# Kernel tuning notes

Measured on AMD Instinct MI355X. Metric: run time of the kernel, lower is better.

The kernel has to match this reference:

```python
import jax, jax.numpy as jnp
import numpy as np

N_PROT = 100_000; E_PROT = 1_600_000
N_LIG = 5_000;    E_LIG = 80_000
B_PROT = 64; B_LIG = 1
SEQ = 130; D = 45; K = 4; DIN = 74
PROT_DIMS = [DIN, 50, 45, 45]
LIG_DIMS  = [DIN, 50, 45, 45, 45]
HEAD = [SEQ * D, 2000, 1000, 500, 1]


def setup_inputs() -> dict:
    key = jax.random.key(0)
    ks = iter(jax.random.split(key, 64))
    def rn(shape, scale=1.0):
        return jax.random.normal(next(ks), shape, jnp.float32) * scale
    inp = {
        "prot_x": rn((N_PROT, DIN)),
        "lig_x": rn((N_LIG, DIN)),
    }
    for pref, dims in (("prot", PROT_DIMS), ("lig", LIG_DIMS)):
        for i in range(len(dims) - 1):
            fan_in = (K + 1) * dims[i]
            inp[f"{pref}_W{i}"] = rn((fan_in, dims[i + 1]), fan_in ** -0.5)
            inp[f"{pref}_b{i}"] = jnp.zeros((dims[i + 1],), jnp.float32)
    inp["qkv_w"] = rn((D, 3 * D), D ** -0.5)
    inp["qkv_b"] = jnp.zeros((3 * D,), jnp.float32)
    inp["proj_w"] = rn((D, D), D ** -0.5)
    inp["proj_b"] = jnp.zeros((D,), jnp.float32)
    for i in range(3):
        inp[f"h{i}_w"] = rn((HEAD[i], HEAD[i + 1]), HEAD[i] ** -0.5)
        inp[f"h{i}_b"] = jnp.zeros((HEAD[i + 1],), jnp.float32)
    inp["fc_w"] = rn((HEAD[3], HEAD[4]), HEAD[3] ** -0.5)
    inp["fc_b"] = jnp.zeros((HEAD[4],), jnp.float32)
    inp["prot_src"] = jax.random.randint(next(ks), (E_PROT,), 0, N_PROT, jnp.int32)
    inp["prot_dst"] = jax.random.randint(next(ks), (E_PROT,), 0, N_PROT, jnp.int32)
    # deterministic contiguous subgraph ids guarantee all 64 pockets are non-empty
    inp["prot_gid"] = (jnp.arange(N_PROT) * B_PROT // N_PROT).astype(jnp.int32)
    inp["lig_src"] = jax.random.randint(next(ks), (E_LIG,), 0, N_LIG, jnp.int32)
    inp["lig_dst"] = jax.random.randint(next(ks), (E_LIG,), 0, N_LIG, jnp.int32)
    inp["lig_gid"] = jnp.zeros((N_LIG,), jnp.int32)
    inp["training"] = 0
    return inp


def _tagconv(x, src, dst, W, b, n):
    # DGL TAGConv: h_{k+1} = D^{-1/2} A D^{-1/2} h_k ; out = [h_0..h_K] @ W + b
    deg = jax.ops.segment_sum(jnp.ones_like(dst, x.dtype), dst, num_segments=n)
    norm = jnp.where(deg > 0, deg, 1.0) ** -0.5  # clamp(min=1)^-0.5
    hops = [x]
    h = x
    for _ in range(K):
        h = norm[:, None] * jax.ops.segment_sum((h * norm[:, None])[src], dst, num_segments=n)
        hops.append(h)
    return jnp.concatenate(hops, axis=-1) @ W + b


def _l2norm(x):
    # F.normalize(dim=1): x / max(||x||_2, eps)
    return x / jnp.maximum(jnp.linalg.norm(x, axis=1, keepdims=True), 1e-12)


def _gnn(x, src, dst, gid, Ws, bs, n, ngraphs):
    for W, b in zip(Ws, bs):
        x = _l2norm(jax.nn.relu(_tagconv(x, src, dst, W, b, n)))
        # dropout is identity in eval mode
    return jax.ops.segment_max(x, gid, num_segments=ngraphs)  # DGL MaxPooling


def reference(prot_x, lig_x,
              prot_W0, prot_b0, prot_W1, prot_b1, prot_W2, prot_b2,
              lig_W0, lig_b0, lig_W1, lig_b1, lig_W2, lig_b2, lig_W3, lig_b3,
              qkv_w, qkv_b, proj_w, proj_b,
              h0_w, h0_b, h1_w, h1_b, h2_w, h2_b, fc_w, fc_b,
              prot_src, prot_dst, prot_gid, lig_src, lig_dst, lig_gid, training):
    prot_rep = _gnn(prot_x, prot_src, prot_dst, prot_gid,
                    [prot_W0, prot_W1, prot_W2], [prot_b0, prot_b1, prot_b2],
                    N_PROT, B_PROT)                    # [B_PROT, 45]
    lig_rep = _gnn(lig_x, lig_src, lig_dst, lig_gid,
                   [lig_W0, lig_W1, lig_W2, lig_W3], [lig_b0, lig_b1, lig_b2, lig_b3],
                   N_LIG, B_LIG)                       # [B_LIG, 45]
    n_seq = B_LIG + B_PROT
    seq = jnp.concatenate([lig_rep, prot_rep], axis=0)  # [n_seq, 45]
    seq = jnp.pad(seq, ((0, SEQ - n_seq), (0, 0)))[None]  # [1, 130, 45]

    # eye-based mask exactly as the torch code builds it
    idx = jnp.arange(SEQ)
    valid = idx < n_seq
    mask = jnp.eye(SEQ, dtype=jnp.float32) * (valid[:, None] & valid[None, :])
    mask = mask.at[:, n_seq - 1].set(1.0)
    mask = mask.at[n_seq - 1, :].set(1.0)
    mask = mask.at[n_seq - 1, n_seq - 1].set(0.0)

    qkv = seq @ qkv_w + qkv_b                 # [1, 130, 135]
    q, k, v = jnp.split(qkv, 3, axis=-1)      # single head, head_dim = 45
    attn = jnp.einsum("bqd,bkd->bqk", q, k) * (D ** -0.5)
    attn = jnp.where(mask[None] == 0, -1e9, attn)
    attn = jax.nn.softmax(attn, axis=-1)
    out = jnp.einsum("bqk,bkd->bqd", attn, v) @ proj_w + proj_b  # [1,130,45]

    out = out.reshape(1, SEQ * D)             # [1, 5850]
    for w, b in ((h0_w, h0_b), (h1_w, h1_b), (h2_w, h2_b)):
        out = jax.nn.relu(out @ w + b)        # head dropout off in eval
    return jax.nn.sigmoid(out @ fc_w + fc_b)  # [1, 1]
```

## Files before the change

### kernel.cpp

```cpp
#include <hip/hip_runtime.h>
#include <hip/hip_fp16.h>
#include <cstddef>
#include <cstdint>

namespace {

constexpr int NPROT = 100000;
constexpr int EPROT = 1600000;
constexpr int NLIG  = 5000;
constexpr int ELIG  = 80000;


__global__ void hist_kernel(const int* __restrict__ dst, int* __restrict__ cnt, int e) {
  int i = blockIdx.x * 256 + threadIdx.x;
  if (i < e) atomicAdd(&cnt[dst[i]], 1);
}

__global__ void scan1_kernel(const int* __restrict__ cnt, int* __restrict__ rp,
                             int* __restrict__ bsum, float* __restrict__ nrm, int n) {
  __shared__ int wsum[4];
  int t = threadIdx.x;
  int base = blockIdx.x * 1024 + t * 4;
  int v0 = 0, v1 = 0, v2 = 0, v3 = 0;
  if (base + 3 < n) {
    int4 val = *(const int4*)(cnt + base);
    v0 = val.x; v1 = val.y; v2 = val.z; v3 = val.w;
  } else if (base < n) {
    v0 = cnt[base];
    if (base + 1 < n) v1 = cnt[base + 1];
    if (base + 2 < n) v2 = cnt[base + 2];
  }
  if (base < n)     nrm[base]     = 1.0f / sqrtf(fmaxf((float)v0, 1.0f));
  if (base + 1 < n) nrm[base + 1] = 1.0f / sqrtf(fmaxf((float)v1, 1.0f));
  if (base + 2 < n) nrm[base + 2] = 1.0f / sqrtf(fmaxf((float)v2, 1.0f));
  if (base + 3 < n) nrm[base + 3] = 1.0f / sqrtf(fmaxf((float)v3, 1.0f));
  int ts = v0 + v1 + v2 + v3;
  int lane = t & 63, wv = t >> 6;
  int incl = ts;
  #pragma unroll
  for (int off = 1; off < 64; off <<= 1) {
    int o = __shfl_up(incl, off, 64);
    if (lane >= off) incl += o;
  }
  if (lane == 63) wsum[wv] = incl;
  __syncthreads();
  int woff = 0;
  #pragma unroll
  for (int i = 0; i < 4; ++i) if (i < wv) woff += wsum[i];
  int excl = woff + incl - ts;
  int o0 = excl, o1 = o0 + v0, o2 = o1 + v1, o3 = o2 + v2;
  if (base + 3 < n) {
    *(int4*)(rp + base) = make_int4(o0, o1, o2, o3);
  } else if (base < n) {
    rp[base] = o0;
    if (base + 1 < n) rp[base + 1] = o1;
    if (base + 2 < n) rp[base + 2] = o2;
  }
  if (t == 255) bsum[blockIdx.x] = woff + incl;
}

__global__ void scan2_kernel(int* __restrict__ bsum, int nb, int* __restrict__ rp_end) {
  __shared__ int s[256];
  int t = threadIdx.x;
  int v = (t < nb) ? bsum[t] : 0;
  s[t] = v;
  __syncthreads();
  int val = v;
  for (int off = 1; off < 256; off <<= 1) {
    int add = (t >= off) ? s[t - off] : 0;
    __syncthreads();
    val += add;
    s[t] = val;
    __syncthreads();
  }
  if (t < nb) bsum[t] = val - v;
  if (t == 255) *rp_end = val;
}

__global__ void scan3_kernel(int* __restrict__ rp, const int* __restrict__ bsum, int n) {
  int i = blockIdx.x * 256 + threadIdx.x;
  if (i < n) rp[i] += bsum[i >> 10];
}

__global__ void scatter_kernel(const int* __restrict__ src, const int* __restrict__ dst,
                               const int* __restrict__ rp, int* __restrict__ cur,
                               int* __restrict__ col, int e) {
  int i = blockIdx.x * 256 + threadIdx.x;
  if (i < e) {
    int d = dst[i];
    int p = rp[d] + atomicAdd(&cur[d], 1);
    col[p] = src[i];
  }
}


__global__ void gather_all_kernel(const __half* __restrict__ gin, const int* __restrict__ rp,
                                  const int* __restrict__ col, const float* __restrict__ nrm,
                                  __half* __restrict__ gout, int n, int nbn) {
  int pass = blockIdx.x / nbn;
  int bid = blockIdx.x - pass * nbn;
  int lane = threadIdx.x & 63, wv = threadIdx.x >> 6;
  int q = lane >> 4, r = lane & 15;
  int e_slot = r >> 3, f2 = r & 7;
  int v = bid * 16 + wv * 4 + q;
  bool vok = (v < n);
  int beg = 0, deg = 0;
  if (vok) { beg = rp[v]; deg = rp[v + 1] - beg; }
  const __half* gc = gin + (size_t)pass * n * 16;
  __half* go = gout + (size_t)pass * n * 16;
  float ax = 0.f, ay = 0.f;
  for (int base = 0; __any(base < deg); base += 16) {
    int ec = (base + r < deg) ? col[beg + base + r] : -1;
    #pragma unroll
    for (int js = 0; js < 16; js += 2) {
      int sl = (q << 4) + js + e_slot;
      int s0 = __shfl(ec, sl, 64);
      int idx = (s0 >= 0) ? s0 : 0;
      float m = (s0 >= 0) ? 1.f : 0.f;
      __half2 h2 = *(const __half2*)(gc + (size_t)idx * 16 + (f2 << 1));
      ax += m * __low2float(h2);
      ay += m * __high2float(h2);
    }
  }
  ax += __shfl_xor(ax, 8, 64);
  ay += __shfl_xor(ay, 8, 64);
  if (vok && e_slot == 0) {
    float nm = nrm[v];
    float nm2 = nm * nm;
    *(__half2*)(go + (size_t)v * 16 + (f2 << 1)) = __floats2half2_rn(ax * nm2, ay * nm2);
  }
}

template<int DIN>
__global__ void init_g0_kernel(const float* __restrict__ x, const float* __restrict__ nrm,
                               __half* __restrict__ g0, int n) {
  constexpr int PD = (DIN + 15) & ~15;
  int lane = threadIdx.x & 63;
  int v = blockIdx.x * 4 + (threadIdx.x >> 6);
  if (v >= n) return;
  float nm = nrm[v];
  for (int f = lane; f < PD; f += 64) {
    float val = (f < DIN) ? x[(size_t)v * DIN + f] * nm : 0.f;
    g0[(((size_t)(f >> 4) * n + v) << 4) + (f & 15)] = __float2half(val);
  }
}

__global__ void padw_kernel(const float* __restrict__ W, float* __restrict__ Wp,
                            int din, int dout, int pd) {
  int i = blockIdx.x * 256 + threadIdx.x;
  int total = 5 * pd * dout;
  if (i >= total) return;
  int f = i / dout, j = i - f * dout;
  int hop = f / pd, rem = f - hop * pd;
  Wp[i] = (rem < din) ? W[(size_t)(hop * din + rem) * dout + j] : 0.f;
}

template<int DIN, int DOUT, bool LAST>
__global__ __launch_bounds__(256) void combine_kernel(
    const __half* __restrict__ gbase, const float* __restrict__ nrm,
    const float* __restrict__ Wp, const float* __restrict__ bias,
    __half* __restrict__ gnext, float* __restrict__ Xout, int n) {
  constexpr int PD = (DIN + 15) & ~15;
  constexpr int NCH = PD / 16;
  constexpr int PDN = (DOUT + 15) & ~15;
  int v = blockIdx.x * 256 + threadIdx.x;
  if (v >= n) return;
  const size_t slabh = (size_t)n * 80;
  float acc[DOUT];
  #pragma unroll
  for (int j = 0; j < DOUT; ++j) acc[j] = 0.f;
  const float* wr = Wp;
  for (int hop = 0; hop < 5; ++hop) {
    const __half* hrow = gbase + (size_t)hop * slabh + ((size_t)v << 4);
    for (int ch = 0; ch < NCH; ++ch) {
      float h[16];
      #pragma unroll
      for (int s2 = 0; s2 < 8; ++s2) {
        __half2 hh = *(const __half2*)(hrow + s2 * 2);
        h[2 * s2]     = __low2float(hh);
        h[2 * s2 + 1] = __high2float(hh);
      }
      #pragma unroll
      for (int s = 0; s < 16; ++s) {
        #pragma unroll
        for (int j = 0; j < DOUT; ++j) acc[j] += h[s] * wr[s * DOUT + j];
      }
      wr += 16 * DOUT;
      hrow += ((size_t)n << 4);
    }
  }
  float rn = 1.f / nrm[v];
  float ss = 0.f;
  #pragma unroll
  for (int j = 0; j < DOUT; ++j) {
    float y = bias[j] + acc[j] * rn;
    y = fmaxf(y, 0.f);
    acc[j] = y;
    ss += y * y;
  }
  float sc = 1.f / fmaxf(sqrtf(ss), 1e-12f);
  if (LAST) {
    #pragma unroll
    for (int j = 0; j < DOUT; ++j) Xout[(size_t)v * DOUT + j] = acc[j] * sc;
  } else {
    float nm = nrm[v];
    #pragma unroll
    for (int ch = 0; ch < PDN / 16; ++ch) {
      __half* go = gnext + (((size_t)ch * n + v) << 4);
      #pragma unroll
      for (int s2 = 0; s2 < 8; ++s2) {
        int j0 = ch * 16 + s2 * 2, j1 = j0 + 1;
        float a = (j0 < DOUT) ? acc[j0] * sc * nm : 0.f;
        float b = (j1 < DOUT) ? acc[j1] * sc * nm : 0.f;
        *(__half2*)(go + s2 * 2) = __floats2half2_rn(a, b);
      }
    }
  }
}


template<int DIN, int GS, int DOUT>
__global__ void init_gemm_kernel(const float* __restrict__ x, const float* __restrict__ nrm,
                                 const float* __restrict__ W, const float* __restrict__ bias,
                                 __half* __restrict__ gout, float* __restrict__ y, int n) {
  int lane = threadIdx.x & 63;
  int v = blockIdx.x * 4 + (threadIdx.x >> 6);
  if (v >= n) return;
  float nm = nrm[v];
  const float* xr = x + (size_t)v * DIN;
  float hA = (lane < DIN) ? xr[lane] : 0.f;
  float hB = 0.f;
  if constexpr (DIN > 64) { if (lane + 64 < DIN) hB = xr[lane + 64]; }
  __half* go = gout + (size_t)v * GS;
  if (lane < DIN) go[lane] = __float2half(hA * nm);
  if constexpr (DIN > 64) { if (lane + 64 < DIN) go[lane + 64] = __float2half(hB * nm); }
  int cl = (lane < DOUT) ? lane : 0;
  float acc = bias[cl];
  const float* Wk = W + cl;
  #pragma unroll
  for (int f = 0; f < DIN; ++f) {
    float hf = (f < 64) ? __shfl(hA, f, 64) : __shfl(hB, f - 64, 64);
    acc += hf * Wk[(size_t)f * DOUT];
  }
  if (lane < DOUT) y[(size_t)v * DOUT + lane] = acc;
}

template<int DIN, int GS, int DOUT, bool WRITEG, bool FINAL>
__global__ void fused_hop_kernel(const __half* __restrict__ gin, const int* __restrict__ rp,
                                 const int* __restrict__ col, const float* __restrict__ nrm,
                                 const float* __restrict__ W, __half* __restrict__ gout,
                                 float* __restrict__ y, float* __restrict__ Xout,
                                 int k, int n) {
  int lane = threadIdx.x & 63;
  int v = blockIdx.x * 4 + (threadIdx.x >> 6);
  if (v >= n) return;
  int beg = rp[v], end = rp[v + 1];
  float a0 = 0.f, a1 = 0.f;
  for (int base = beg; base < end; base += 64) {
    int m = end - base; if (m > 64) m = 64;
    int myc = (lane < m) ? col[base + lane] : 0;
    int j = 0;
    for (; j + 8 <= m; j += 8) {
      int ss[8];
      float t0[8], t1[8];
      #pragma unroll
      for (int u = 0; u < 8; ++u) ss[u] = __shfl(myc, j + u, 64);
      #pragma unroll
      for (int u = 0; u < 8; ++u) {
        const __half* rr = gin + (size_t)ss[u] * GS;
        t0[u] = (lane < DIN) ? __half2float(rr[lane]) : 0.f;
        if constexpr (DIN > 64) t1[u] = (lane + 64 < DIN) ? __half2float(rr[lane + 64]) : 0.f;
      }
      #pragma unroll
      for (int u = 0; u < 8; ++u) {
        a0 += t0[u];
        if constexpr (DIN > 64) a1 += t1[u];
      }
    }
    for (; j < m; ++j) {
      int s = __shfl(myc, j, 64);
      const __half* rr = gin + (size_t)s * GS;
      if (lane < DIN) a0 += __half2float(rr[lane]);
      if constexpr (DIN > 64) { if (lane + 64 < DIN) a1 += __half2float(rr[lane + 64]); }
    }
  }
  float nm = nrm[v];
  float hA = a0 * nm, hB = a1 * nm;
  if (WRITEG) {
    __half* go = gout + (size_t)v * GS;
    if (lane < DIN) go[lane] = __float2half(hA * nm);
    if constexpr (DIN > 64) { if (lane + 64 < DIN) go[lane + 64] = __float2half(hB * nm); }
  }
  int cl = (lane < DOUT) ? lane : 0;
  float acc = 0.f;
  if (lane < DOUT) acc = y[(size_t)v * DOUT + lane];
  const float* Wk = W + (size_t)k * DIN * DOUT + cl;
  #pragma unroll
  for (int f = 0; f < DIN; ++f) {
    float hf = (f < 64) ? __shfl(hA, f, 64) : __shfl(hB, f - 64, 64);
    acc += hf * Wk[(size_t)f * DOUT];
  }
  if constexpr (FINAL) {
    float val = (lane < DOUT) ? fmaxf(acc, 0.f) : 0.f;
    float ss2 = val * val;
    #pragma unroll
    for (int off2 = 32; off2 > 0; off2 >>= 1) ss2 += __shfl_xor(ss2, off2, 64);
    float scale = 1.f / fmaxf(sqrtf(ss2), 1e-12f);
    if (lane < DOUT) Xout[(size_t)v * DOUT + lane] = val * scale;
  } else {
    if (lane < DOUT) y[(size_t)v * DOUT + lane] = acc;
  }
}

__global__ void segmax_kernel(const float* __restrict__ X, const int* __restrict__ gid,
                              float* __restrict__ rep, int n, int row_off) {
  __shared__ float tab[4][45];
  __shared__ int gids[256];
  int t = threadIdx.x;
  for (int i = t; i < 4 * 45; i += 256) ((float*)tab)[i] = 0.f;
  int v0 = blockIdx.x * 256;
  int vend = v0 + 256; if (vend > n) vend = n;
  int nv = vend - v0;
  if (t < nv) gids[t] = gid[v0 + t];
  __syncthreads();
  int g0 = gids[0];
  int total = nv * 45;
  for (int i = t; i < total; i += 256) {
    int vl = i / 45, j = i - vl * 45;
    float val = X[(size_t)(v0 + vl) * 45 + j];
    int rel = gids[vl] - g0;
    if (rel >= 0 && rel < 4)
      atomicMax((unsigned int*)&tab[rel][j], __float_as_uint(val));
    else
      atomicMax((unsigned int*)&rep[(size_t)(row_off + gids[vl]) * 45 + j], __float_as_uint(val));
  }
  __syncthreads();
  for (int i = t; i < 4 * 45; i += 256) {
    float val = ((float*)tab)[i];
    if (val > 0.f) {
      int rel = i / 45, j = i - rel * 45;
      atomicMax((unsigned int*)&rep[(size_t)(row_off + g0 + rel) * 45 + j], __float_as_uint(val));
    }
  }
}


__global__ void qkv_kernel(const float* __restrict__ rep, const float* __restrict__ w,
                           const float* __restrict__ b, float* __restrict__ qkv) {
  int i = blockIdx.x;
  int t = threadIdx.x;
  __shared__ float sr[45];
  if (t < 45) sr[t] = (i < 65) ? rep[(size_t)i * 45 + t] : 0.f;
  __syncthreads();
  if (t < 135) {
    float acc = b[t];
    #pragma unroll 5
    for (int d = 0; d < 45; ++d) acc += sr[d] * w[d * 135 + t];
    qkv[(size_t)i * 135 + t] = acc;
  }
}

__global__ void attn_kernel(const float* __restrict__ qkv, const float* __restrict__ proj_w,
                            const float* __restrict__ proj_b, float* __restrict__ ctx) {
  int i = blockIdx.x;
  int t = threadIdx.x;
  __shared__ float q[45];
  __shared__ float p[130];
  __shared__ float red[256];
  __shared__ float ao[45];
  if (t < 45) q[t] = qkv[(size_t)i * 135 + t];
  __syncthreads();
  float s = -1e30f;
  if (t < 130) {
    int j = t;
    float dot = 0.f;
    #pragma unroll 5
    for (int d = 0; d < 45; ++d) dot += q[d] * qkv[(size_t)j * 135 + 45 + d];
    dot *= 0.14907119849998599f;
    bool mz;
    if (i == 64 && j == 64) mz = true;
    else if (i == 64 || j == 64) mz = false;
    else mz = !(i == j && i < 65);
    s = mz ? -1e9f : dot;
  }
  red[t] = s;
  __syncthreads();
  #pragma unroll
  for (int off = 128; off > 0; off >>= 1) {
    if (t < off) red[t] = fmaxf(red[t], red[t + off]);
    __syncthreads();
  }
  float mx = red[0];
  __syncthreads();
  float e = (t < 130) ? expf(s - mx) : 0.f;
  red[t] = e;
  __syncthreads();
  #pragma unroll
  for (int off = 128; off > 0; off >>= 1) {
    if (t < off) red[t] += red[t + off];
    __syncthreads();
  }
  float denom = red[0];
  __syncthreads();
  if (t < 130) p[t] = e / denom;
  __syncthreads();
  if (t < 45) {
    float acc = 0.f;
    for (int j = 0; j < 130; ++j) acc += p[j] * qkv[(size_t)j * 135 + 90 + t];
    ao[t] = acc;
  }
  __syncthreads();
  if (t < 45) {
    float pr = proj_b[t];
    #pragma unroll 5
    for (int e2 = 0; e2 < 45; ++e2) pr += ao[e2] * proj_w[e2 * 45 + t];
    ctx[(size_t)i * 45 + t] = pr;
  }
}


__global__ void bias_init_kernel(const float* __restrict__ b, float* __restrict__ out, int n) {
  int i = blockIdx.x * 256 + threadIdx.x;
  if (i < n) out[i] = b[i];
}

template<bool RELU_IN>
__global__ void fc_splitk_kernel(const float* __restrict__ x, const float* __restrict__ W,
                                 float* __restrict__ out, int nin, int nout, int kchunk) {
  __shared__ float xs[1024];
  int k0 = blockIdx.y * kchunk;
  int k1 = k0 + kchunk; if (k1 > nin) k1 = nin;
  int len = k1 - k0;
  for (int i = threadIdx.x; i < len; i += blockDim.x) {
    float v = x[k0 + i];
    xs[i] = RELU_IN ? fmaxf(v, 0.f) : v;
  }
  __syncthreads();
  int j = blockIdx.x * blockDim.x + threadIdx.x;
  if (j < nout) {
    float acc = 0.f;
    const float* Wp = W + (size_t)k0 * nout + j;
    for (int i = 0; i < len; ++i) acc += xs[i] * Wp[(size_t)i * nout];
    atomicAdd(&out[j], acc);
  }
}

__global__ void final_fc_kernel(const float* __restrict__ x, const float* __restrict__ W,
                                const float* __restrict__ b, float* __restrict__ out) {
  __shared__ float red[512];
  int t = threadIdx.x;
  float acc = 0.f;
  if (t < 500) acc = fmaxf(x[t], 0.f) * W[t];
  red[t] = acc;
  __syncthreads();
  #pragma unroll
  for (int off = 256; off > 0; off >>= 1) {
    if (t < off) red[t] += red[t + off];
    __syncthreads();
  }
  if (t == 0) {
    float z = red[0] + b[0];
    out[0] = 1.f / (1.f + expf(-z));
  }
}


struct Bufs {
  __half* slabs;
  __half *ligA, *ligB;
  float *X, *Y, *nrm, *Wp;
  int *cnt, *cur, *rp, *col, *bsum;
};

template<int DIN, int DOUT, bool LAST>
void run_layer_prot(const Bufs& g, const float* W, const float* b, int n, hipStream_t st) {
  constexpr int PD = (DIN + 15) & ~15;
  constexpr int NPASS = PD / 16;
  int nbn = (n + 15) / 16;
  size_t slabh = (size_t)n * 80;
  for (int k = 1; k <= 4; ++k)
    gather_all_kernel<<<NPASS * nbn, 256, 0, st>>>(g.slabs + (size_t)(k - 1) * slabh,
                                                   g.rp, g.col, g.nrm,
                                                   g.slabs + (size_t)k * slabh, n, nbn);
  int wtotal = 5 * PD * DOUT;
  padw_kernel<<<(wtotal + 255) / 256, 256, 0, st>>>(W, g.Wp, DIN, DOUT, PD);
  combine_kernel<DIN, DOUT, LAST><<<(n + 255) / 256, 256, 0, st>>>(
      g.slabs, g.nrm, g.Wp, b, g.slabs, g.X, n);
}

template<int DIN, int GS, int DOUT>
void run_layer_lig(const float* xin, const Bufs& g, const float* W, const float* b,
                   int n, hipStream_t st) {
  int nb = (n + 3) / 4;
  init_gemm_kernel<DIN, GS, DOUT><<<nb, 256, 0, st>>>(xin, g.nrm, W, b, g.ligA, g.Y, n);
  const __half* gin = g.ligA;
  __half* gout = g.ligB;
  for (int k = 1; k <= 4; ++k) {
    if (k < 4)
      fused_hop_kernel<DIN, GS, DOUT, true, false><<<nb, 256, 0, st>>>(gin, g.rp, g.col, g.nrm, W, gout, g.Y, g.X, k, n);
    else
      fused_hop_kernel<DIN, GS, DOUT, false, true><<<nb, 256, 0, st>>>(gin, g.rp, g.col, g.nrm, W, gout, g.Y, g.X, 4, n);
    __half* t = (__half*)gin; gin = gout; gout = t;
  }
}

void build_csr(const int* src, const int* dst, const Bufs& g, int n, int e, hipStream_t st) {
  hipMemsetAsync(g.cnt, 0, (size_t)n * 4, st);
  hipMemsetAsync(g.cur, 0, (size_t)n * 4, st);
  hist_kernel<<<(e + 255) / 256, 256, 0, st>>>(dst, g.cnt, e);
  int nb1 = (n + 1023) / 1024;
  scan1_kernel<<<nb1, 256, 0, st>>>(g.cnt, g.rp, g.bsum, g.nrm, n);
  scan2_kernel<<<1, 256, 0, st>>>(g.bsum, nb1, g.rp + n);
  scan3_kernel<<<(n + 255) / 256, 256, 0, st>>>(g.rp, g.bsum, n);
  scatter_kernel<<<(e + 255) / 256, 256, 0, st>>>(src, dst, g.rp, g.cur, g.col, e);
}

}

extern "C" void kernel_launch(void* const* d_in, const int* in_sizes, int n_in,
                              void* d_out, int out_size, void* d_ws, size_t ws_size,
                              hipStream_t stream) {
  (void)in_sizes; (void)n_in; (void)out_size;

  const float* prot_x = (const float*)d_in[0];
  const float* lig_x  = (const float*)d_in[1];
  const float* pW[3] = {(const float*)d_in[2], (const float*)d_in[4], (const float*)d_in[6]};
  const float* pB[3] = {(const float*)d_in[3], (const float*)d_in[5], (const float*)d_in[7]};
  const float* lW[4] = {(const float*)d_in[8], (const float*)d_in[10], (const float*)d_in[12], (const float*)d_in[14]};
  const float* lB[4] = {(const float*)d_in[9], (const float*)d_in[11], (const float*)d_in[13], (const float*)d_in[15]};
  const float* qkv_w = (const float*)d_in[16];
  const float* qkv_b = (const float*)d_in[17];
  const float* proj_w = (const float*)d_in[18];
  const float* proj_b = (const float*)d_in[19];
  const float* h0_w = (const float*)d_in[20];
  const float* h0_b = (const float*)d_in[21];
  const float* h1_w = (const float*)d_in[22];
  const float* h1_b = (const float*)d_in[23];
  const float* h2_w = (const float*)d_in[24];
  const float* h2_b = (const float*)d_in[25];
  const float* fc_w = (const float*)d_in[26];
  const float* fc_b = (const float*)d_in[27];
  const int* prot_src = (const int*)d_in[28];
  const int* prot_dst = (const int*)d_in[29];
  const int* prot_gid = (const int*)d_in[30];
  const int* lig_src  = (const int*)d_in[31];
  const int* lig_dst  = (const int*)d_in[32];
  const int* lig_gid  = (const int*)d_in[33];

  char* w = (char*)d_ws;
  size_t off = 0;
  auto alloc = [&](size_t bytes) -> void* {
    void* p = w + off;
    off += (bytes + 255) & ~(size_t)255;
    return p;
  };
  __half* slabs = (__half*)alloc((size_t)5 * NPROT * 80 * 2);
  __half* ligA  = (__half*)alloc((size_t)NLIG * 96 * 2);
  __half* ligB  = (__half*)alloc((size_t)NLIG * 96 * 2);
  float* X   = (float*)alloc((size_t)NPROT * 45 * 4);
  float* Y   = (float*)alloc((size_t)NLIG * 50 * 4);
  float* nrm = (float*)alloc((size_t)NPROT * 4);
  float* Wp  = (float*)alloc((size_t)5 * 80 * 50 * 4);
  int* cnt   = (int*)alloc((size_t)NPROT * 4);
  int* cur   = (int*)alloc((size_t)NPROT * 4);
  int* rp    = (int*)alloc(((size_t)NPROT + 1) * 4);
  int* colb  = (int*)alloc((size_t)EPROT * 4);
  int* bsum  = (int*)alloc((size_t)256 * 4);
  float* rep = (float*)alloc((size_t)65 * 45 * 4);
  float* qkvb = (float*)alloc((size_t)130 * 135 * 4);
  float* ctx  = (float*)alloc((size_t)5850 * 4);
  float* hb0  = (float*)alloc((size_t)2000 * 4);
  float* hb1  = (float*)alloc((size_t)1000 * 4);
  float* hb2  = (float*)alloc((size_t)500 * 4);
  if (off > ws_size) return;

  hipMemsetAsync(rep, 0, (size_t)65 * 45 * 4, stream);

  Bufs g{slabs, ligA, ligB, X, Y, nrm, Wp, cnt, cur, rp, colb, bsum};

  build_csr(prot_src, prot_dst, g, NPROT, EPROT, stream);
  init_g0_kernel<74><<<(NPROT + 3) / 4, 256, 0, stream>>>(prot_x, g.nrm, g.slabs, NPROT);
  run_layer_prot<74, 50, false>(g, pW[0], pB[0], NPROT, stream);
  run_layer_prot<50, 45, false>(g, pW[1], pB[1], NPROT, stream);
  run_layer_prot<45, 45, true >(g, pW[2], pB[2], NPROT, stream);
  segmax_kernel<<<(NPROT + 255) / 256, 256, 0, stream>>>(g.X, prot_gid, rep, NPROT, 1);

  build_csr(lig_src, lig_dst, g, NLIG, ELIG, stream);
  run_layer_lig<74, 96, 50>(lig_x, g, lW[0], lB[0], NLIG, stream);
  run_layer_lig<50, 64, 45>(g.X, g, lW[1], lB[1], NLIG, stream);
  run_layer_lig<45, 64, 45>(g.X, g, lW[2], lB[2], NLIG, stream);
  run_layer_lig<45, 64, 45>(g.X, g, lW[3], lB[3], NLIG, stream);
  segmax_kernel<<<(NLIG + 255) / 256, 256, 0, stream>>>(g.X, lig_gid, rep, NLIG, 0);

  qkv_kernel<<<130, 256, 0, stream>>>(rep, qkv_w, qkv_b, qkvb);
  attn_kernel<<<130, 256, 0, stream>>>(qkvb, proj_w, proj_b, ctx);

  bias_init_kernel<<<8, 256, 0, stream>>>(h0_b, hb0, 2000);
  fc_splitk_kernel<false><<<dim3(8, 8), 256, 0, stream>>>(ctx, h0_w, hb0, 5850, 2000, 732);
  bias_init_kernel<<<4, 256, 0, stream>>>(h1_b, hb1, 1000);
  fc_splitk_kernel<true><<<dim3(4, 4), 256, 0, stream>>>(hb0, h1_w, hb1, 2000, 1000, 500);
  bias_init_kernel<<<2, 256, 0, stream>>>(h2_b, hb2, 500);
  fc_splitk_kernel<true><<<dim3(2, 2), 256, 0, stream>>>(hb1, h2_w, hb2, 1000, 500, 500);
  final_fc_kernel<<<1, 512, 0, stream>>>(hb2, fc_w, fc_b, (float*)d_out);
}
```

Baseline: 1.542 ms.

## Split combine output columns across waves and widen gather loads

The protein combine kernel now gives each node to four waves, each computing a quarter of the output columns. The L2-norm sum of squares is reduced through shared memory, which cuts per-thread accumulator registers and raises occupancy. The gather kernel switches from half2 to 8-byte loads, with four features per lane and four edge slots, plus an extra shuffle stage in the reduction. Each node's h rows are now read four times, once per wave, and the weight buffer gets padding for overrun reads.

```diff
diff --git a/kernel.cpp b/kernel.cpp
--- a/kernel.cpp
+++ b/kernel.cpp
@@ -94,6 +94,11 @@
 }
 
 
+__device__ __forceinline__ float2 cvt_h2(uint32_t u) {
+  __half2 h = *reinterpret_cast<__half2*>(&u);
+  return make_float2(__low2float(h), __high2float(h));
+}
+
 __global__ void gather_all_kernel(const __half* __restrict__ gin, const int* __restrict__ rp,
                                   const int* __restrict__ col, const float* __restrict__ nrm,
                                   __half* __restrict__ gout, int n, int nbn) {
@@ -101,33 +106,40 @@
   int bid = blockIdx.x - pass * nbn;
   int lane = threadIdx.x & 63, wv = threadIdx.x >> 6;
   int q = lane >> 4, r = lane & 15;
-  int e_slot = r >> 3, f2 = r & 7;
+  int e_slot = r >> 2, f4 = r & 3;
   int v = bid * 16 + wv * 4 + q;
   bool vok = (v < n);
   int beg = 0, deg = 0;
   if (vok) { beg = rp[v]; deg = rp[v + 1] - beg; }
   const __half* gc = gin + (size_t)pass * n * 16;
   __half* go = gout + (size_t)pass * n * 16;
-  float ax = 0.f, ay = 0.f;
+  float a0 = 0.f, a1 = 0.f, a2 = 0.f, a3 = 0.f;
   for (int base = 0; __any(base < deg); base += 16) {
     int ec = (base + r < deg) ? col[beg + base + r] : -1;
     #pragma unroll
-    for (int js = 0; js < 16; js += 2) {
+    for (int js = 0; js < 16; js += 4) {
       int sl = (q << 4) + js + e_slot;
       int s0 = __shfl(ec, sl, 64);
       int idx = (s0 >= 0) ? s0 : 0;
       float m = (s0 >= 0) ? 1.f : 0.f;
-      __half2 h2 = *(const __half2*)(gc + (size_t)idx * 16 + (f2 << 1));
-      ax += m * __low2float(h2);
-      ay += m * __high2float(h2);
-    }
-  }
-  ax += __shfl_xor(ax, 8, 64);
-  ay += __shfl_xor(ay, 8, 64);
+      uint2 u = *(const uint2*)(gc + (size_t)idx * 16 + (f4 << 2));
+      float2 p0 = cvt_h2(u.x), p1 = cvt_h2(u.y);
+      a0 += m * p0.x; a1 += m * p0.y; a2 += m * p1.x; a3 += m * p1.y;
+    }
+  }
+  a0 += __shfl_xor(a0, 4, 64);  a1 += __shfl_xor(a1, 4, 64);
+  a2 += __shfl_xor(a2, 4, 64);  a3 += __shfl_xor(a3, 4, 64);
+  a0 += __shfl_xor(a0, 8, 64);  a1 += __shfl_xor(a1, 8, 64);
+  a2 += __shfl_xor(a2, 8, 64);  a3 += __shfl_xor(a3, 8, 64);
   if (vok && e_slot == 0) {
     float nm = nrm[v];
     float nm2 = nm * nm;
-    *(__half2*)(go + (size_t)v * 16 + (f2 << 1)) = __floats2half2_rn(ax * nm2, ay * nm2);
+    __half2 w0 = __floats2half2_rn(a0 * nm2, a1 * nm2);
+    __half2 w1 = __floats2half2_rn(a2 * nm2, a3 * nm2);
+    uint2 st;
+    st.x = *reinterpret_cast<uint32_t*>(&w0);
+    st.y = *reinterpret_cast<uint32_t*>(&w1);
+    *(uint2*)(go + ((size_t)v << 4) + (f4 << 2)) = st;
   }
 }
 
@@ -160,59 +172,83 @@
     const __half* __restrict__ gbase, const float* __restrict__ nrm,
     const float* __restrict__ Wp, const float* __restrict__ bias,
     __half* __restrict__ gnext, float* __restrict__ Xout, int n) {
-  constexpr int PD = (DIN + 15) & ~15;
+  constexpr int PD  = (DIN + 15) & ~15;
   constexpr int NCH = PD / 16;
   constexpr int PDN = (DOUT + 15) & ~15;
-  int v = blockIdx.x * 256 + threadIdx.x;
-  if (v >= n) return;
+  constexpr int QO  = ((DOUT + 7) / 8) * 2;
+  __shared__ float ssq[4 * 64];
+  int lane = threadIdx.x & 63, wv = threadIdx.x >> 6;
+  int v = blockIdx.x * 64 + lane;
+  bool vok = (v < n);
+  int vc = vok ? v : 0;
   const size_t slabh = (size_t)n * 80;
-  float acc[DOUT];
-  #pragma unroll
-  for (int j = 0; j < DOUT; ++j) acc[j] = 0.f;
-  const float* wr = Wp;
+  int cofs = __builtin_amdgcn_readfirstlane(wv) * QO;
+  float acc[QO];
+  #pragma unroll
+  for (int jj = 0; jj < QO; ++jj) acc[jj] = 0.f;
+  const float* wb = Wp + cofs;
   for (int hop = 0; hop < 5; ++hop) {
-    const __half* hrow = gbase + (size_t)hop * slabh + ((size_t)v << 4);
+    const __half* hrow = gbase + (size_t)hop * slabh + ((size_t)vc << 4);
+    #pragma unroll 1
     for (int ch = 0; ch < NCH; ++ch) {
+      uint4 u0 = *(const uint4*)hrow;
+      uint4 u1 = *(const uint4*)(hrow + 8);
       float h[16];
-      #pragma unroll
-      for (int s2 = 0; s2 < 8; ++s2) {
-        __half2 hh = *(const __half2*)(hrow + s2 * 2);
-        h[2 * s2]     = __low2float(hh);
-        h[2 * s2 + 1] = __high2float(hh);
+      {
+        float2 p;
+        p = cvt_h2(u0.x); h[0] = p.x; h[1] = p.y;
+        p = cvt_h2(u0.y); h[2] = p.x; h[3] = p.y;
+        p = cvt_h2(u0.z); h[4] = p.x; h[5] = p.y;
+        p = cvt_h2(u0.w); h[6] = p.x; h[7] = p.y;
+        p = cvt_h2(u1.x); h[8] = p.x; h[9] = p.y;
+        p = cvt_h2(u1.y); h[10] = p.x; h[11] = p.y;
+        p = cvt_h2(u1.z); h[12] = p.x; h[13] = p.y;
+        p = cvt_h2(u1.w); h[14] = p.x; h[15] = p.y;
       }
       #pragma unroll
       for (int s = 0; s < 16; ++s) {
         #pragma unroll
-        for (int j = 0; j < DOUT; ++j) acc[j] += h[s] * wr[s * DOUT + j];
+        for (int jj = 0; jj < QO; ++jj) acc[jj] += h[s] * wb[s * DOUT + jj];
       }
-      wr += 16 * DOUT;
+      wb += 16 * DOUT;
       hrow += ((size_t)n << 4);
     }
   }
-  float rn = 1.f / nrm[v];
+  float rn = 1.f / nrm[vc];
   float ss = 0.f;
   #pragma unroll
-  for (int j = 0; j < DOUT; ++j) {
-    float y = bias[j] + acc[j] * rn;
-    y = fmaxf(y, 0.f);
-    acc[j] = y;
+  for (int jj = 0; jj < QO; ++jj) {
+    int j = cofs + jj;
+    float y = (j < DOUT) ? fmaxf(bias[j] + acc[jj] * rn, 0.f) : 0.f;
+    acc[jj] = y;
     ss += y * y;
   }
-  float sc = 1.f / fmaxf(sqrtf(ss), 1e-12f);
+  ssq[wv * 64 + lane] = ss;
+  __syncthreads();
+  if (!vok) return;
+  float tot = ssq[lane] + ssq[64 + lane] + ssq[128 + lane] + ssq[192 + lane];
+  float sc = 1.f / fmaxf(sqrtf(tot), 1e-12f);
   if (LAST) {
     #pragma unroll
-    for (int j = 0; j < DOUT; ++j) Xout[(size_t)v * DOUT + j] = acc[j] * sc;
+    for (int jj = 0; jj < QO; ++jj) {
+      int j = cofs + jj;
+      if (j < DOUT) Xout[(size_t)v * DOUT + j] = acc[jj] * sc;
+    }
   } else {
     float nm = nrm[v];
     #pragma unroll
-    for (int ch = 0; ch < PDN / 16; ++ch) {
-      __half* go = gnext + (((size_t)ch * n + v) << 4);
+    for (int jj = 0; jj < QO; jj += 2) {
+      int j0 = cofs + jj;
+      float a = (j0 < DOUT) ? acc[jj] * sc * nm : 0.f;
+      float b = (j0 + 1 < DOUT) ? acc[jj + 1] * sc * nm : 0.f;
+      int ch = j0 >> 4, s = j0 & 15;
+      *(__half2*)(gnext + (((size_t)ch * n + v) << 4) + s) = __floats2half2_rn(a, b);
+    }
+    if (wv == 3) {
       #pragma unroll
-      for (int s2 = 0; s2 < 8; ++s2) {
-        int j0 = ch * 16 + s2 * 2, j1 = j0 + 1;
-        float a = (j0 < DOUT) ? acc[j0] * sc * nm : 0.f;
-        float b = (j1 < DOUT) ? acc[j1] * sc * nm : 0.f;
-        *(__half2*)(go + s2 * 2) = __floats2half2_rn(a, b);
+      for (int j0 = 4 * QO; j0 < PDN; j0 += 2) {
+        int ch = j0 >> 4, s = j0 & 15;
+        *(__half2*)(gnext + (((size_t)ch * n + v) << 4) + s) = __floats2half2_rn(0.f, 0.f);
       }
     }
   }
@@ -484,7 +520,7 @@
                                                    g.slabs + (size_t)k * slabh, n, nbn);
   int wtotal = 5 * PD * DOUT;
   padw_kernel<<<(wtotal + 255) / 256, 256, 0, st>>>(W, g.Wp, DIN, DOUT, PD);
-  combine_kernel<DIN, DOUT, LAST><<<(n + 255) / 256, 256, 0, st>>>(
+  combine_kernel<DIN, DOUT, LAST><<<(n + 63) / 64, 256, 0, st>>>(
       g.slabs, g.nrm, g.Wp, b, g.slabs, g.X, n);
 }
 
@@ -560,7 +596,7 @@
   float* X   = (float*)alloc((size_t)NPROT * 45 * 4);
   float* Y   = (float*)alloc((size_t)NLIG * 50 * 4);
   float* nrm = (float*)alloc((size_t)NPROT * 4);
-  float* Wp  = (float*)alloc((size_t)5 * 80 * 50 * 4);
+  float* Wp  = (float*)alloc((size_t)5 * 80 * 50 * 4 + 256);
   int* cnt   = (int*)alloc((size_t)NPROT * 4);
   int* cur   = (int*)alloc((size_t)NPROT * 4);
   int* rp    = (int*)alloc(((size_t)NPROT + 1) * 4);
```

Result: faster. 1.422 ms (-7.8%).
